# Kernel tuning notes

Hardware: AMD Instinct MI355X
Metric: run time of the kernel (lower is better)

The kernel has to match this reference:

```python
import jax, jax.numpy as jnp
import numpy as np

TAU = 0.5
BETA = 10.0
NUM_NODES = 200000
NUM_EDGES = 200000
NODE_DIM = 128
EDGE_DIM = 128
D = 16
GROUPS = {4: 12000, 8: 6000}


def setup_inputs() -> dict:
    key = jax.random.key(0)
    ks = jax.random.split(key, 8)
    inp = {
        "n": jax.random.normal(ks[0], (NUM_NODES, NODE_DIM), dtype=jnp.float32),
        "e": jax.random.normal(ks[1], (NUM_EDGES, EDGE_DIM), dtype=jnp.float32),
        "W": jax.random.normal(ks[2], (1, NODE_DIM, EDGE_DIM), dtype=jnp.float32) * 0.02,
        "b": jnp.zeros((1,), dtype=jnp.float32),
        "hypernode_k4": jax.random.randint(ks[3], (GROUPS[4],), 0, NUM_NODES),
        "hyperedge_k4": jax.random.randint(ks[4], (GROUPS[4], 4, D), 0, NUM_EDGES),
        "hypernode_k8": jax.random.randint(ks[5], (GROUPS[8],), 0, NUM_NODES),
        "hyperedge_k8": jax.random.randint(ks[6], (GROUPS[8], 8, D), 0, NUM_EDGES),
    }
    return inp


def _group_loss(n, e, W, b, node_idx, edge_idx, k):
    # node_idx: [N], edge_idx: [N, k, D]
    t = n[node_idx] @ W[0]                       # [N, E] anchor projected through bilinear weight
    ce = e[edge_idx]                             # [N, k, D, E] gathered contrast edges
    logits = jnp.einsum('ne,nkde->nkd', t, ce) + b[0]
    s = jnp.exp(jax.nn.sigmoid(logits) / TAU).sum(-1)   # [N, k] score_list
    suffix = jnp.cumsum(s[:, ::-1], axis=1)[:, ::-1]    # suffix sums s[:, j:].sum
    ratio = s[:, : k - 1] / suffix[:, : k - 1]
    return (-jnp.log(jnp.minimum(ratio, BETA))).sum(axis=1) / (k - 1)  # [N]


def reference(n, e, W, b, hypernode_k4, hyperedge_k4, hypernode_k8, hyperedge_k8):
    l4 = _group_loss(n, e, W, b, hypernode_k4, hyperedge_k4, 4)
    l8 = _group_loss(n, e, W, b, hypernode_k8, hyperedge_k8, 8)
    return jnp.concatenate([l4, l8]).mean()
```

## Files before the change

kernel.cpp:

```cpp
#include <hip/hip_runtime.h>
#include <hip/hip_bf16.h>

#define N4 12000
#define N8 6000
#define NTOT 18000
#define NBLK (NTOT / 4)
#define NK8BLK (N8 / 4)
#define NE 200000

#define NTBLK  1125
#define NEBLK  6250
#define TSTRIDE 5
#define PREP_GRID (NTBLK + NEBLK)

#if __has_builtin(__builtin_amdgcn_sdot4)
#define USE_SDOT4 1
#else
#define USE_SDOT4 0
#endif

#if __has_builtin(__builtin_amdgcn_sched_barrier)
#define SCHED_FENCE() __builtin_amdgcn_sched_barrier(0)
#else
#define SCHED_FENCE()
#endif

#define OFF_PART  256
#define PART_B    (NBLK * 4)
#define OFF_T8    ((OFF_PART + PART_B + 255) & ~255)
#define T8_B      (NTOT * 128)
#define OFF_E8    ((OFF_T8 + T8_B + 255) & ~255)
#define M_MIN     16384

#define E_SCALE   30.0f
#define T_SCALE   110.0f
#define INV_SCALE (1.0f / (E_SCALE * T_SCALE))

template<bool BF16>
__device__ __forceinline__ float loadf(const void* p, long i) {
    if constexpr (BF16) {
        unsigned short v = ((const unsigned short*)p)[i];
        return __uint_as_float(((unsigned int)v) << 16);
    } else {
        return ((const float*)p)[i];
    }
}

template<bool BF16>
__device__ __forceinline__ void loadpair(const void* p, long pairIdx, float& a, float& b) {
    if constexpr (BF16) {
        unsigned int u = ((const unsigned int*)p)[pairIdx];
        a = __uint_as_float(u << 16);
        b = __uint_as_float(u & 0xffff0000u);
    } else {
        float2 v = ((const float2*)p)[pairIdx];
        a = v.x; b = v.y;
    }
}

__device__ __forceinline__ int qb(float x, float s) {
    return (int)rintf(fminf(fmaxf(x * s, -127.0f), 127.0f));
}

__device__ __forceinline__ unsigned int q4(const float* f, float s) {
    unsigned int r = 0;
#pragma unroll
    for (int q = 0; q < 4; q++)
        r |= ((unsigned int)qb(f[q], s) & 0xffu) << (8 * q);
    return r;
}

__device__ __forceinline__ int dot4i(unsigned int a, unsigned int b, int c) {
#if USE_SDOT4
    return __builtin_amdgcn_sdot4((int)a, (int)b, c, false);
#else
#pragma unroll
    for (int q = 0; q < 4; q++) {
        int av = ((int)(a << ((3 - q) * 8))) >> 24;
        int bv = ((int)(b << ((3 - q) * 8))) >> 24;
        c += av * bv;
    }
    return c;
#endif
}

__device__ __forceinline__ bool detect_bf16(const void* W) {
    const unsigned short* u = (const unsigned short*)W;
    const int lane = threadIdx.x & 63;
    bool wild = false;
#pragma unroll
    for (int q = 0; q < 4; q++) {
        float f = __uint_as_float(((unsigned int)u[lane * 4 + q]) << 16);
        if (!(fabsf(f) < 1.0f)) wild = true;
    }
    return __ballot(wild) == 0ull;
}

__device__ __forceinline__ int heavy_first(int b) {
    return (b < NK8BLK) ? (b + (N4 / 4)) : (b - NK8BLK);
}

template<bool BF16>
__device__ __forceinline__ void t4_body(int lane, float* nl, int rbase,
                                        const void* n, const void* W,
                                        const int* hn4, const int* hn8,
                                        unsigned char* t8) {
    float a0[4], a1[4];
#pragma unroll
    for (int r = 0; r < 4; r++) {
        int row = rbase + r;
        int node = (row < N4) ? hn4[row] : hn8[row - N4];
        long nb = (long)node * 128;
        a0[r] = loadf<BF16>(n, nb + lane);
        a1[r] = loadf<BF16>(n, nb + 64 + lane);
    }
    ((float4*)nl)[lane]      = make_float4(a0[0], a0[1], a0[2], a0[3]);
    ((float4*)nl)[lane + 64] = make_float4(a1[0], a1[1], a1[2], a1[3]);

    float t0[4] = {0, 0, 0, 0}, t1[4] = {0, 0, 0, 0};
#pragma unroll 8
    for (int c = 0; c < 128; c++) {
        float4 nc = ((const float4*)nl)[c];
        float w0, w1;
        loadpair<BF16>(W, (long)c * 64 + lane, w0, w1);
        t0[0] = fmaf(nc.x, w0, t0[0]); t1[0] = fmaf(nc.x, w1, t1[0]);
        t0[1] = fmaf(nc.y, w0, t0[1]); t1[1] = fmaf(nc.y, w1, t1[1]);
        t0[2] = fmaf(nc.z, w0, t0[2]); t1[2] = fmaf(nc.z, w1, t1[2]);
        t0[3] = fmaf(nc.w, w0, t0[3]); t1[3] = fmaf(nc.w, w1, t1[3]);
    }
#pragma unroll
    for (int r = 0; r < 4; r++) {
        int b0 = qb(t0[r], T_SCALE), b1 = qb(t1[r], T_SCALE);
        ((unsigned short*)(t8 + (long)(rbase + r) * 128))[lane] =
            (unsigned short)((b0 & 0xff) | ((b1 & 0xff) << 8));
    }
}

__global__ __launch_bounds__(256) void k_prep(
    const void* n, const void* e, const void* W,
    const int* hn4, const int* hn8,
    unsigned char* t8, uint4* e8, int tmode)
{
    const bool bf = detect_bf16(W);
    const int b = blockIdx.x;

    bool is_t = false;
    int tb = 0, eb = 0;
    if (tmode) {
        if (b < NTBLK * TSTRIDE) {
            if (b % TSTRIDE == 0) { is_t = true; tb = b / TSTRIDE; }
            else                  { eb = b - b / TSTRIDE - 1; }
        } else {
            eb = b - NTBLK;
        }
    } else {
        if (b < NTBLK) { is_t = true; tb = b; }
        else           { eb = b - NTBLK; }
    }

    if (is_t) {
        __shared__ __align__(16) float nl4[4][512];
        const int lane = threadIdx.x & 63, wave = threadIdx.x >> 6;
        const int rbase = (tb * 4 + wave) * 4;
        if (bf) t4_body<true >(lane, nl4[wave], rbase, n, W, hn4, hn8, t8);
        else    t4_body<false>(lane, nl4[wave], rbase, n, W, hn4, hn8, t8);
    } else {
        long gid = (long)eb * 256 + threadIdx.x;
        float f[16];
        if (bf) {
            const uint4* p = ((const uint4*)e) + gid * 2;
            uint4 a = p[0], bb = p[1];
            const unsigned int w[8] = {a.x, a.y, a.z, a.w, bb.x, bb.y, bb.z, bb.w};
#pragma unroll
            for (int q = 0; q < 8; q++) {
                f[2 * q]     = __uint_as_float(w[q] << 16);
                f[2 * q + 1] = __uint_as_float(w[q] & 0xffff0000u);
            }
        } else {
            const float4* p = ((const float4*)e) + gid * 4;
#pragma unroll
            for (int q = 0; q < 4; q++) {
                float4 x = p[q];
                f[4 * q] = x.x; f[4 * q + 1] = x.y; f[4 * q + 2] = x.z; f[4 * q + 3] = x.w;
            }
        }
        e8[gid] = make_uint4(q4(f, E_SCALE), q4(f + 4, E_SCALE),
                             q4(f + 8, E_SCALE), q4(f + 12, E_SCALE));
    }
}

template<int K, bool FULL>
__device__ __forceinline__ float row_body(
    int lane, int row, const int* ebase,
    const void* e, const unsigned char* e8, const unsigned char* t8,
    long M, float bval, bool bf)
{
    const int sub = lane & 7, grp = lane >> 3;
    constexpr int NCH = K * 2;

    int idx[NCH];
    {
        const int4* ip = (const int4*)(ebase + grp * NCH);
#pragma unroll
        for (int q = 0; q < NCH / 4; q++) {
            int4 v = ip[q];
            idx[4 * q] = v.x; idx[4 * q + 1] = v.y; idx[4 * q + 2] = v.z; idx[4 * q + 3] = v.w;
        }
    }

    uint4 tqv = *(const uint4*)(t8 + (long)row * 128 + sub * 16);

    uint4 buf[NCH];
#pragma unroll
    for (int i = 0; i < NCH; i++) {
        if (FULL || idx[i] < M)
            buf[i] = *(const uint4*)(e8 + (unsigned int)idx[i] * 128u + sub * 16);
    }
    SCHED_FENCE();

    float sacc = 0.0f;
#pragma unroll
    for (int ch = 0; ch < NCH; ch++) {
        uint4 v = buf[ch];
        if (!FULL && idx[ch] >= M) {
            float ev[16];
            long eidx = idx[ch];
            if (bf) {
                const uint4* p = (const uint4*)(((const unsigned short*)e) + eidx * 128 + sub * 16);
                uint4 a = p[0], bb = p[1];
                const unsigned int w[8] = {a.x, a.y, a.z, a.w, bb.x, bb.y, bb.z, bb.w};
#pragma unroll
                for (int q = 0; q < 8; q++) {
                    ev[2 * q]     = __uint_as_float(w[q] << 16);
                    ev[2 * q + 1] = __uint_as_float(w[q] & 0xffff0000u);
                }
            } else {
                const float4* p = (const float4*)(((const float*)e) + eidx * 128 + sub * 16);
#pragma unroll
                for (int q = 0; q < 4; q++) {
                    float4 x = p[q];
                    ev[4 * q] = x.x; ev[4 * q + 1] = x.y; ev[4 * q + 2] = x.z; ev[4 * q + 3] = x.w;
                }
            }
            v.x = q4(ev, E_SCALE); v.y = q4(ev + 4, E_SCALE);
            v.z = q4(ev + 8, E_SCALE); v.w = q4(ev + 12, E_SCALE);
        }

        int d = 0;
        d = dot4i(v.x, tqv.x, d);
        d = dot4i(v.y, tqv.y, d);
        d = dot4i(v.z, tqv.z, d);
        d = dot4i(v.w, tqv.w, d);
        float dotf = (float)d * INV_SCALE;

        dotf += __shfl_xor(dotf, 1);
        dotf += __shfl_xor(dotf, 2);
        dotf += __shfl_xor(dotf, 4);

        float logit = dotf + bval;
        float sig = 1.0f / (1.0f + __expf(-logit));
        sacc += __expf(sig * 2.0f);
    }

    float s_all[K];
#pragma unroll
    for (int j = 0; j < K; j++) {
        if constexpr (K == 4) s_all[j] = __shfl(sacc, j * 16) + __shfl(sacc, j * 16 + 8);
        else                  s_all[j] = __shfl(sacc, j * 8);
    }

    float lsum = 0.0f;
    if (lane == 0) {
        float suffix = s_all[K - 1];
#pragma unroll
        for (int j = K - 2; j >= 0; j--) {
            suffix += s_all[j];
            float ratio = fminf(s_all[j] / suffix, 10.0f);
            lsum += -__logf(ratio);
        }
        lsum /= (float)(K - 1);
    }
    return lsum;
}

template<bool FULL>
__global__ __launch_bounds__(256) void k_main(
    const void* e, const unsigned char* e8, const unsigned char* t8, long M,
    const void* W, const void* bptr,
    const int* he4, const int* he8, float* part)
{
    __shared__ float wsum[4];
    const int lane = threadIdx.x & 63, wave = threadIdx.x >> 6;
    const int blk = heavy_first(blockIdx.x);
    const int row = blk * 4 + wave;
    const bool bf = detect_bf16(W);
    const float bval = bf ? loadf<true>(bptr, 0) : loadf<false>(bptr, 0);

    float lsum;
    if (row < N4) {
        lsum = row_body<4, FULL>(lane, row, he4 + (long)row * 64, e, e8, t8, M, bval, bf);
    } else {
        int r = row - N4;
        lsum = row_body<8, FULL>(lane, row, he8 + (long)r * 128, e, e8, t8, M, bval, bf);
    }
    if (lane == 0) wsum[wave] = lsum;
    __syncthreads();
    if (threadIdx.x == 0) part[blockIdx.x] = wsum[0] + wsum[1] + wsum[2] + wsum[3];
}

__global__ __launch_bounds__(256) void k_sumpart(const float* part, const void* W, void* out) {
    __shared__ float ws[4];
    const int tid = threadIdx.x;
    const bool bf = detect_bf16(W);
    float v = 0.0f;
    for (int i = tid; i < NBLK; i += 256) v += part[i];
    v += __shfl_xor(v,1); v += __shfl_xor(v,2); v += __shfl_xor(v,4);
    v += __shfl_xor(v,8); v += __shfl_xor(v,16); v += __shfl_xor(v,32);
    if ((tid & 63) == 0) ws[tid >> 6] = v;
    __syncthreads();
    if (tid == 0) {
        float m = (ws[0]+ws[1]+ws[2]+ws[3]) / (float)NTOT;
        if (bf) ((__hip_bfloat16*)out)[0] = __float2bfloat16(m);
        else    ((float*)out)[0] = m;
    }
}

extern "C" void kernel_launch(void* const* d_in, const int* in_sizes, int n_in,
                              void* d_out, int out_size, void* d_ws, size_t ws_size,
                              hipStream_t stream) {
    const void* n    = d_in[0];
    const void* e    = d_in[1];
    const void* W    = d_in[2];
    const void* bptr = d_in[3];
    const int* hn4 = (const int*)d_in[4];
    const int* he4 = (const int*)d_in[5];
    const int* hn8 = (const int*)d_in[6];
    const int* he8 = (const int*)d_in[7];

    char* ws = (char*)d_ws;
    float* part = (float*)(ws + OFF_PART);
    unsigned char* t8 = (unsigned char*)(ws + OFF_T8);
    unsigned char* e8 = (unsigned char*)(ws + OFF_E8);

    long M = 0;
    if (ws_size >= (size_t)OFF_E8 + (size_t)M_MIN * 128) {
        M = (long)((ws_size - OFF_E8) / 128);
        if (M > NE) M = NE;
        M &= ~31L;
    }

    if (M >= NE) {
        k_prep<<<PREP_GRID, 256, 0, stream>>>(n, e, W, hn4, hn8, t8, (uint4*)e8, 1);
        k_main<true ><<<NBLK, 256, 0, stream>>>(e, e8, t8, (long)NE, W, bptr, he4, he8, part);
    } else {
        int neblk = (int)(M / 32);
        k_prep<<<NTBLK + neblk, 256, 0, stream>>>(n, e, W, hn4, hn8, t8, (uint4*)e8, 0);
        k_main<false><<<NBLK, 256, 0, stream>>>(e, e8, t8, M, W, bptr, he4, he8, part);
    }
    k_sumpart<<<1, 256, 0, stream>>>(part, W, d_out);
}
```

Before: 250.5 us.

## Split prep into separate anchor-projection and edge-quantize kernels with LDS-staged W

The fused prep kernel, which interleaved anchor-projection blocks with edge-quantization blocks, is split into two launches. The projection kernel stages W in shared memory as packed bf16 (converting from fp32 if needed), and each wave now processes 8 rows instead of 4 so W is reused more. The edge quantization kernel now has each thread handle 4 elements per iteration with coalesced stride access. This removes repeated global W reads but adds a kernel launch and drops the overlap of the two workloads, and rounding W to bf16 may slightly change fp32 results.

Result: slower. 262.0 us (+4.6%).

```diff
diff --git a/kernel.cpp b/kernel.cpp
--- a/kernel.cpp
+++ b/kernel.cpp
@@ -8,10 +8,9 @@
 #define NK8BLK (N8 / 4)
 #define NE 200000
 
-#define NTBLK  1125
+#define NT2BLK 563
 #define NEBLK  6250
-#define TSTRIDE 5
-#define PREP_GRID (NTBLK + NEBLK)
+#define PREP_E_TILE 4096
 
 #if __has_builtin(__builtin_amdgcn_sdot4)
 #define USE_SDOT4 1
@@ -46,18 +45,6 @@
     }
 }
 
-template<bool BF16>
-__device__ __forceinline__ void loadpair(const void* p, long pairIdx, float& a, float& b) {
-    if constexpr (BF16) {
-        unsigned int u = ((const unsigned int*)p)[pairIdx];
-        a = __uint_as_float(u << 16);
-        b = __uint_as_float(u & 0xffff0000u);
-    } else {
-        float2 v = ((const float2*)p)[pairIdx];
-        a = v.x; b = v.y;
-    }
-}
-
 __device__ __forceinline__ int qb(float x, float s) {
     return (int)rintf(fminf(fmaxf(x * s, -127.0f), 127.0f));
 }
@@ -101,28 +88,31 @@
 }
 
 template<bool BF16>
-__device__ __forceinline__ void t4_body(int lane, float* nl, int rbase,
-                                        const void* n, const void* W,
-                                        const int* hn4, const int* hn8,
-                                        unsigned char* t8) {
+__device__ __forceinline__ void t_group(
+    int lane, float4* nst, int rbase,
+    const void* n, const unsigned int* Wl,
+    const int* hn4, const int* hn8, unsigned char* t8)
+{
     float a0[4], a1[4];
 #pragma unroll
     for (int r = 0; r < 4; r++) {
         int row = rbase + r;
-        int node = (row < N4) ? hn4[row] : hn8[row - N4];
+        int rr = (row < NTOT) ? row : (NTOT - 1);
+        int node = (rr < N4) ? hn4[rr] : hn8[rr - N4];
         long nb = (long)node * 128;
         a0[r] = loadf<BF16>(n, nb + lane);
         a1[r] = loadf<BF16>(n, nb + 64 + lane);
     }
-    ((float4*)nl)[lane]      = make_float4(a0[0], a0[1], a0[2], a0[3]);
-    ((float4*)nl)[lane + 64] = make_float4(a1[0], a1[1], a1[2], a1[3]);
+    nst[lane]      = make_float4(a0[0], a0[1], a0[2], a0[3]);
+    nst[lane + 64] = make_float4(a1[0], a1[1], a1[2], a1[3]);
 
     float t0[4] = {0, 0, 0, 0}, t1[4] = {0, 0, 0, 0};
 #pragma unroll 8
     for (int c = 0; c < 128; c++) {
-        float4 nc = ((const float4*)nl)[c];
-        float w0, w1;
-        loadpair<BF16>(W, (long)c * 64 + lane, w0, w1);
+        float4 nc = nst[c];
+        unsigned int w = Wl[c * 64 + lane];
+        float w0 = __uint_as_float(w << 16);
+        float w1 = __uint_as_float(w & 0xffff0000u);
         t0[0] = fmaf(nc.x, w0, t0[0]); t1[0] = fmaf(nc.x, w1, t1[0]);
         t0[1] = fmaf(nc.y, w0, t0[1]); t1[1] = fmaf(nc.y, w1, t1[1]);
         t0[2] = fmaf(nc.z, w0, t0[2]); t1[2] = fmaf(nc.z, w1, t1[2]);
@@ -130,62 +120,73 @@
     }
 #pragma unroll
     for (int r = 0; r < 4; r++) {
-        int b0 = qb(t0[r], T_SCALE), b1 = qb(t1[r], T_SCALE);
-        ((unsigned short*)(t8 + (long)(rbase + r) * 128))[lane] =
-            (unsigned short)((b0 & 0xff) | ((b1 & 0xff) << 8));
-    }
-}
-
-__global__ __launch_bounds__(256) void k_prep(
-    const void* n, const void* e, const void* W,
-    const int* hn4, const int* hn8,
-    unsigned char* t8, uint4* e8, int tmode)
-{
+        int row = rbase + r;
+        if (row < NTOT) {
+            int b0 = qb(t0[r], T_SCALE), b1 = qb(t1[r], T_SCALE);
+            ((unsigned short*)(t8 + (long)row * 128))[lane] =
+                (unsigned short)((b0 & 0xff) | ((b1 & 0xff) << 8));
+        }
+    }
+}
+
+__global__ __launch_bounds__(256) void k_prep_t(
+    const void* n, const void* W,
+    const int* hn4, const int* hn8, unsigned char* t8)
+{
+    __shared__ __align__(16) unsigned int Wl[8192];
+    __shared__ __align__(16) float4 nst[4 * 128];
     const bool bf = detect_bf16(W);
-    const int b = blockIdx.x;
-
-    bool is_t = false;
-    int tb = 0, eb = 0;
-    if (tmode) {
-        if (b < NTBLK * TSTRIDE) {
-            if (b % TSTRIDE == 0) { is_t = true; tb = b / TSTRIDE; }
-            else                  { eb = b - b / TSTRIDE - 1; }
+    const int tid = threadIdx.x;
+    const int lane = tid & 63, wave = tid >> 6;
+
+    if (bf) {
+        const unsigned int* Wp = (const unsigned int*)W;
+#pragma unroll 8
+        for (int i = 0; i < 32; i++) {
+            int s = tid + i * 256;
+            Wl[s] = Wp[s];
+        }
+    } else {
+        const float2* Wp = (const float2*)W;
+#pragma unroll 8
+        for (int i = 0; i < 32; i++) {
+            int s = tid + i * 256;
+            float2 v = Wp[s];
+            __hip_bfloat16 h0 = __float2bfloat16(v.x), h1 = __float2bfloat16(v.y);
+            Wl[s] = (unsigned int)*(unsigned short*)&h0 |
+                    ((unsigned int)*(unsigned short*)&h1 << 16);
+        }
+    }
+    __syncthreads();
+
+    const int rw = (blockIdx.x * 4 + wave) * 8;
+    if (bf) {
+        t_group<true >(lane, nst + wave * 128, rw,     n, Wl, hn4, hn8, t8);
+        t_group<true >(lane, nst + wave * 128, rw + 4, n, Wl, hn4, hn8, t8);
+    } else {
+        t_group<false>(lane, nst + wave * 128, rw,     n, Wl, hn4, hn8, t8);
+        t_group<false>(lane, nst + wave * 128, rw + 4, n, Wl, hn4, hn8, t8);
+    }
+}
+
+__global__ __launch_bounds__(256) void k_prep_e(const void* e, const void* W, unsigned int* e8)
+{
+    const bool bf = detect_bf16(W);
+    const int tid = threadIdx.x;
+    const long base = (long)blockIdx.x * 1024;
+#pragma unroll
+    for (int q = 0; q < 4; q++) {
+        long s = base + q * 256 + tid;
+        float f[4];
+        if (bf) {
+            uint2 u = ((const uint2*)e)[s];
+            f[0] = __uint_as_float(u.x << 16); f[1] = __uint_as_float(u.x & 0xffff0000u);
+            f[2] = __uint_as_float(u.y << 16); f[3] = __uint_as_float(u.y & 0xffff0000u);
         } else {
-            eb = b - NTBLK;
-        }
-    } else {
-        if (b < NTBLK) { is_t = true; tb = b; }
-        else           { eb = b - NTBLK; }
-    }
-
-    if (is_t) {
-        __shared__ __align__(16) float nl4[4][512];
-        const int lane = threadIdx.x & 63, wave = threadIdx.x >> 6;
-        const int rbase = (tb * 4 + wave) * 4;
-        if (bf) t4_body<true >(lane, nl4[wave], rbase, n, W, hn4, hn8, t8);
-        else    t4_body<false>(lane, nl4[wave], rbase, n, W, hn4, hn8, t8);
-    } else {
-        long gid = (long)eb * 256 + threadIdx.x;
-        float f[16];
-        if (bf) {
-            const uint4* p = ((const uint4*)e) + gid * 2;
-            uint4 a = p[0], bb = p[1];
-            const unsigned int w[8] = {a.x, a.y, a.z, a.w, bb.x, bb.y, bb.z, bb.w};
-#pragma unroll
-            for (int q = 0; q < 8; q++) {
-                f[2 * q]     = __uint_as_float(w[q] << 16);
-                f[2 * q + 1] = __uint_as_float(w[q] & 0xffff0000u);
-            }
-        } else {
-            const float4* p = ((const float4*)e) + gid * 4;
-#pragma unroll
-            for (int q = 0; q < 4; q++) {
-                float4 x = p[q];
-                f[4 * q] = x.x; f[4 * q + 1] = x.y; f[4 * q + 2] = x.z; f[4 * q + 3] = x.w;
-            }
-        }
-        e8[gid] = make_uint4(q4(f, E_SCALE), q4(f + 4, E_SCALE),
-                             q4(f + 8, E_SCALE), q4(f + 12, E_SCALE));
+            float4 v = ((const float4*)e)[s];
+            f[0] = v.x; f[1] = v.y; f[2] = v.z; f[3] = v.w;
+        }
+        e8[s] = q4(f, E_SCALE);
     }
 }
 
@@ -349,12 +350,15 @@
         M &= ~31L;
     }
 
+    k_prep_t<<<NT2BLK, 256, 0, stream>>>(n, W, hn4, hn8, t8);
+
     if (M >= NE) {
-        k_prep<<<PREP_GRID, 256, 0, stream>>>(n, e, W, hn4, hn8, t8, (uint4*)e8, 1);
+        k_prep_e<<<NEBLK, 256, 0, stream>>>(e, W, (unsigned int*)e8);
         k_main<true ><<<NBLK, 256, 0, stream>>>(e, e8, t8, (long)NE, W, bptr, he4, he8, part);
     } else {
         int neblk = (int)(M / 32);
-        k_prep<<<NTBLK + neblk, 256, 0, stream>>>(n, e, W, hn4, hn8, t8, (uint4*)e8, 0);
+        if (neblk > 0)
+            k_prep_e<<<neblk, 256, 0, stream>>>(e, W, (unsigned int*)e8);
         k_main<false><<<NBLK, 256, 0, stream>>>(e, e8, t8, M, W, bptr, he4, he8, part);
     }
     k_sumpart<<<1, 256, 0, stream>>>(part, W, d_out);
```
